# Optimization experiments

Hardware: AMD Instinct MI355X
Metric: run time of the kernel (lower is better)

## Reference

```python
import jax, jax.numpy as jnp
import numpy as np
import math

N = 16384
IN_F = 256
OUT_F = 64
EPS = 1e-6


def setup_inputs() -> dict:
    key = jax.random.key(0)
    k1, k2, k3, k4 = jax.random.split(key, 4)
    stdv = 1.0 / math.sqrt(OUT_F)
    inp = jax.random.normal(k1, (N, IN_F), dtype=jnp.float32)
    adj = jax.random.uniform(k2, (N, N), dtype=jnp.float32)
    weight = jax.random.uniform(k3, (IN_F, OUT_F), dtype=jnp.float32, minval=-stdv, maxval=stdv)
    bias = jax.random.uniform(k4, (OUT_F,), dtype=jnp.float32, minval=-stdv, maxval=stdv)
    return {"input": inp, "adj": adj, "weight": weight, "bias": bias, "p": 2}


def reference(input, adj, weight, bias, p):
    # support: [N, OUT_F]
    support = input @ weight
    mu = jnp.min(support)  # global scalar min
    pre_sup = support - mu + EPS  # >= EPS, safe for pow
    pre_top = pre_sup ** (p + 1)
    pre_down = pre_sup ** p
    # p-power mean aggregation: two adj matmuls sharing adj reads
    output = (adj @ pre_top) / (adj @ pre_down) + mu
    return output + bias
```

## Files before the change

### kernel.cpp

```cpp
#include <hip/hip_runtime.h>
#include <hip/hip_bf16.h>

typedef __attribute__((ext_vector_type(8))) short short8;
typedef __attribute__((ext_vector_type(4))) float f32x4;
typedef unsigned short u16;
typedef unsigned int u32;

#define NROWS 16384
#define KDIM 16384
#define EPS 1e-6f

__device__ __forceinline__ u16 f2bf(float x) {
    union { float f; u32 u; } v; v.f = x;
    u32 u = v.u;
    u32 r = (u + 0x7FFFu + ((u >> 16) & 1u)) >> 16;
    return (u16)r;
}

__device__ __forceinline__ void glds16(const void* g, void* l) {
    __builtin_amdgcn_global_load_lds(
        (const __attribute__((address_space(1))) void*)g,
        (__attribute__((address_space(3))) void*)l, 16, 0, 0);
}

__device__ __forceinline__ short cvbf(float x) {
    __hip_bfloat16 h = __float2bfloat16(x);
    return *(short*)&h;
}

__device__ __forceinline__ short8 cvt8(float4 a, float4 b) {
    short8 r = { cvbf(a.x), cvbf(a.y), cvbf(a.z), cvbf(a.w),
                 cvbf(b.x), cvbf(b.y), cvbf(b.z), cvbf(b.w) };
    return r;
}

__global__ __launch_bounds__(256) void wt_kernel(const float* __restrict__ W,
                                                 float* __restrict__ Wt) {
    int idx = blockIdx.x * 256 + threadIdx.x;
    int k = idx >> 6, c = idx & 63;
    Wt[c * 256 + k] = W[idx];
}

__global__ __launch_bounds__(256) void support_kernel(
    const float* __restrict__ inp, const float* __restrict__ Wt,
    float* __restrict__ sup)
{
    int tid = threadIdx.x;
    int col = tid & 63;
    int rr = tid >> 6;
    int rowbase = blockIdx.x * 32 + rr * 8;
    const float4* wt4 = (const float4*)(Wt + (size_t)col * 256);
    float acc[8];
#pragma unroll
    for (int i = 0; i < 8; ++i) acc[i] = 0.f;
    for (int k4 = 0; k4 < 64; ++k4) {
        float4 wv = wt4[k4];
#pragma unroll
        for (int i = 0; i < 8; ++i) {
            float4 iv = *((const float4*)(inp + (size_t)(rowbase + i) * 256) + k4);
            acc[i] += iv.x * wv.x + iv.y * wv.y + iv.z * wv.z + iv.w * wv.w;
        }
    }
#pragma unroll
    for (int i = 0; i < 8; ++i)
        sup[(size_t)(rowbase + i) * 64 + col] = acc[i];
}

__global__ __launch_bounds__(256) void min_part_kernel(
    const float* __restrict__ sup, float* __restrict__ partmin)
{
    __shared__ float wmin[4];
    int tid = threadIdx.x;
    const float4* s4 = (const float4*)sup;
    size_t idx = (size_t)blockIdx.x * 256 + tid;
    float m = 3.4e38f;
#pragma unroll
    for (int j = 0; j < 4; ++j) {
        float4 v = s4[idx + (size_t)j * 65536];
        m = fminf(m, fminf(fminf(v.x, v.y), fminf(v.z, v.w)));
    }
#pragma unroll
    for (int off = 32; off; off >>= 1) m = fminf(m, __shfl_down(m, off, 64));
    if ((tid & 63) == 0) wmin[tid >> 6] = m;
    __syncthreads();
    if (tid == 0)
        partmin[blockIdx.x] = fminf(fminf(wmin[0], wmin[1]), fminf(wmin[2], wmin[3]));
}

__global__ __launch_bounds__(256) void min_final_kernel(
    const float* __restrict__ partmin, float* __restrict__ mu)
{
    __shared__ float wmin[4];
    int tid = threadIdx.x;
    float m = partmin[tid];
#pragma unroll
    for (int off = 32; off; off >>= 1) m = fminf(m, __shfl_down(m, off, 64));
    if ((tid & 63) == 0) wmin[tid >> 6] = m;
    __syncthreads();
    if (tid == 0)
        mu[0] = fminf(fminf(wmin[0], wmin[1]), fminf(wmin[2], wmin[3]));
}

__global__ __launch_bounds__(256) void build_bt_kernel(
    const float* __restrict__ sup, const float* __restrict__ muptr,
    const int* __restrict__ pptr, u16* __restrict__ Bt)
{
    int k = blockIdx.x * 256 + threadIdx.x;
    float mu = *muptr;
    int p = *pptr;
    const float4* srow = (const float4*)(sup + (size_t)k * 64);
#pragma unroll
    for (int j = 0; j < 16; ++j) {
        float4 v = srow[j];
        float ss[4] = {v.x, v.y, v.z, v.w};
#pragma unroll
        for (int q = 0; q < 4; ++q) {
            int c = j * 4 + q;
            float s = ss[q] - mu + EPS;
            float d = 1.f;
            for (int i = 0; i < p; ++i) d *= s;
            Bt[(size_t)c * KDIM + k] = f2bf(d * s);
            Bt[(size_t)(c + 64) * KDIM + k] = f2bf(d);
        }
    }
}

#define BM 64
#define BN 128
#define BK 64
#define KH 8192
#define NTI 128

__global__ __launch_bounds__(512, 4) void gemm_kernel(
    const float* __restrict__ adj, const u16* __restrict__ Bt,
    float* __restrict__ Pp)
{
    __shared__ __align__(16) float Ash[2][BM * BK];
    __shared__ __align__(16) u16  Bsh[2][BN * BK];

    const int tid = threadIdx.x;
    const int rb = blockIdx.x >> 1;
    const int h  = blockIdx.x & 1;
    const size_t rowbase = (size_t)rb * BM;
    const size_t kbase = (size_t)h * KH;

    const int ga0 = tid,        ga1 = tid + 512;
    const int ar0 = ga0 >> 4,   ax0 = (ga0 & 15) ^ (ar0 & 7);
    const int ar1 = ga1 >> 4,   ax1 = (ga1 & 15) ^ (ar1 & 7);
    const float* asrc0 = adj + (rowbase + ar0) * KDIM + kbase + ax0 * 4;
    const float* asrc1 = adj + (rowbase + ar1) * KDIM + kbase + ax1 * 4;
    const int bn0 = ga0 >> 3,   bx0 = (ga0 & 7) ^ (bn0 & 7);
    const int bn1 = ga1 >> 3,   bx1 = (ga1 & 7) ^ (bn1 & 7);
    const u16* bsrc0 = Bt + (size_t)bn0 * KDIM + kbase + bx0 * 8;
    const u16* bsrc1 = Bt + (size_t)bn1 * KDIM + kbase + bx1 * 8;

    const int lane = tid & 63;
    const int w    = tid >> 6;
    const int wm   = w >> 1;
    const int wn   = w & 1;
    const int l15  = lane & 15, lg = lane >> 4;
    const int arow = wm * 16 + l15;
    const int asw  = arow & 7;

    f32x4 acc[4];
#pragma unroll
    for (int j = 0; j < 4; ++j) acc[j] = (f32x4){0.f, 0.f, 0.f, 0.f};

    auto stage = [&](int kt, int buf) {
        const int koff = kt * BK;
        char* ab = (char*)Ash[buf];
        char* bb = (char*)Bsh[buf];
        glds16(asrc0 + koff, ab + ga0 * 16);
        glds16(asrc1 + koff, ab + ga1 * 16);
        glds16(bsrc0 + koff, bb + ga0 * 16);
        glds16(bsrc1 + koff, bb + ga1 * 16);
    };

    stage(0, 0);

    for (int t = 0; t < NTI; ++t) {
        __syncthreads();
        if (t + 1 < NTI) stage(t + 1, (t + 1) & 1);
        const float4* As4 = (const float4*)Ash[t & 1];
        const short8* Bs8 = (const short8*)Bsh[t & 1];
#pragma unroll
        for (int ks = 0; ks < 2; ++ks) {
            const int x0 = ks * 8 + lg * 2;
            float4 fa = As4[arow * 16 + ((x0    ) ^ asw)];
            float4 fb = As4[arow * 16 + ((x0 + 1) ^ asw)];
            short8 a = cvt8(fa, fb);
            const int bx = ks * 4 + lg;
#pragma unroll
            for (int j = 0; j < 4; ++j) {
                const int n = wn * 32 + (j & 1) * 16 + (j >> 1) * 64 + l15;
                short8 b = Bs8[n * 8 + (bx ^ (n & 7))];
                acc[j] = __builtin_amdgcn_mfma_f32_16x16x32_bf16(a, b, acc[j], 0, 0, 0);
            }
        }
    }

    float* pb = Pp + (size_t)blockIdx.x * (BM * BN);
#pragma unroll
    for (int j = 0; j < 2; ++j) {
#pragma unroll
        for (int q = 0; q < 4; ++q) {
            int r = wm * 16 + lg * 4 + q;
            int c = wn * 32 + j * 16 + l15;
            pb[r * BN + c]      = acc[j][q];
            pb[r * BN + c + 64] = acc[j + 2][q];
        }
    }
}

__global__ __launch_bounds__(256) void reduce_kernel(
    const float* __restrict__ Pp, const float* __restrict__ bias,
    const float* __restrict__ muptr, float* __restrict__ out)
{
    int idx = blockIdx.x * 256 + threadIdx.x;
    int r = idx >> 6, c = idx & 63;
    int rb = r >> 6, rr = r & 63;
    const float* p0 = Pp + (size_t)(rb * 2) * (BM * BN) + rr * BN + c;
    const float* p1 = p0 + BM * BN;
    float T = p0[0]  + p1[0];
    float D = p0[64] + p1[64];
    out[idx] = T / D + muptr[0] + bias[c];
}

extern "C" void kernel_launch(void* const* d_in, const int* in_sizes, int n_in,
                              void* d_out, int out_size, void* d_ws, size_t ws_size,
                              hipStream_t stream)
{
    const float* inp  = (const float*)d_in[0];
    const float* adj  = (const float*)d_in[1];
    const float* W    = (const float*)d_in[2];
    const float* bias = (const float*)d_in[3];
    const int*   p    = (const int*)d_in[4];
    float* out = (float*)d_out;

    char* ws = (char*)d_ws;
    u16*   Bt      = (u16*)ws;
    float* partmin = (float*)(ws + (size_t)4 * 1024 * 1024);
    float* mu      = partmin + 256;
    float* Wt      = (float*)(ws + (size_t)4 * 1024 * 1024 + 4096);
    float* Pp      = (float*)(ws + (size_t)8 * 1024 * 1024);

    float* sup = out;

    wt_kernel       <<<64,   256, 0, stream>>>(W, Wt);
    support_kernel  <<<512,  256, 0, stream>>>(inp, Wt, sup);
    min_part_kernel <<<256,  256, 0, stream>>>(sup, partmin);
    min_final_kernel<<<1,    256, 0, stream>>>(partmin, mu);
    build_bt_kernel <<<64,   256, 0, stream>>>(sup, mu, p, Bt);
    gemm_kernel     <<<512,  512, 0, stream>>>(adj, Bt, Pp);
    reduce_kernel   <<<4096, 256, 0, stream>>>(Pp, bias, mu, out);
}
```

Before: 290.9 us.

## Enlarge GEMM row tile to 128 with 4 waves each computing 32x128

The adj GEMM now uses 128-row tiles with 256 threads per block, and each wave computes two 16-row fragments across all 128 B columns. This reuses each B fragment for two MFMAs and halves how often B is reloaded from global memory across blocks. The launch drops to 256 blocks of 256 threads, one per CU at most, which lowers occupancy and latency hiding on a kernel dominated by streaming adj. The partial-output layout and the reduce kernel are rewritten to index by row and K-half.

```diff
diff --git a/kernel.cpp b/kernel.cpp
--- a/kernel.cpp
+++ b/kernel.cpp
@@ -125,13 +125,13 @@
     }
 }
 
-#define BM 64
+#define BM 128
 #define BN 128
 #define BK 64
 #define KH 8192
 #define NTI 128
 
-__global__ __launch_bounds__(512, 4) void gemm_kernel(
+__global__ __launch_bounds__(256, 1) void gemm_kernel(
     const float* __restrict__ adj, const u16* __restrict__ Bt,
     float* __restrict__ Pp)
 {
@@ -139,41 +139,53 @@
     __shared__ __align__(16) u16  Bsh[2][BN * BK];
 
     const int tid = threadIdx.x;
-    const int rb = blockIdx.x >> 1;
+    const int rg = blockIdx.x >> 1;
     const int h  = blockIdx.x & 1;
-    const size_t rowbase = (size_t)rb * BM;
-    const size_t kbase = (size_t)h * KH;
-
-    const int ga0 = tid,        ga1 = tid + 512;
-    const int ar0 = ga0 >> 4,   ax0 = (ga0 & 15) ^ (ar0 & 7);
-    const int ar1 = ga1 >> 4,   ax1 = (ga1 & 15) ^ (ar1 & 7);
-    const float* asrc0 = adj + (rowbase + ar0) * KDIM + kbase + ax0 * 4;
-    const float* asrc1 = adj + (rowbase + ar1) * KDIM + kbase + ax1 * 4;
-    const int bn0 = ga0 >> 3,   bx0 = (ga0 & 7) ^ (bn0 & 7);
-    const int bn1 = ga1 >> 3,   bx1 = (ga1 & 7) ^ (bn1 & 7);
-    const u16* bsrc0 = Bt + (size_t)bn0 * KDIM + kbase + bx0 * 8;
-    const u16* bsrc1 = Bt + (size_t)bn1 * KDIM + kbase + bx1 * 8;
+    const size_t rowbase = (size_t)rg * BM;
+    const size_t kbase   = (size_t)h * KH;
+
+    const float* asp[8];
+#pragma unroll
+    for (int j = 0; j < 8; ++j) {
+        const int g = tid + j * 256;
+        const int ar = g >> 4;
+        const int ax = (g & 15) ^ (ar & 7);
+        asp[j] = adj + (rowbase + ar) * KDIM + kbase + ax * 4;
+    }
+    const u16* bsp[4];
+#pragma unroll
+    for (int j = 0; j < 4; ++j) {
+        const int g = tid + j * 256;
+        const int bn = g >> 3;
+        const int bx = (g & 7) ^ (bn & 7);
+        bsp[j] = Bt + (size_t)bn * KDIM + kbase + bx * 8;
+    }
 
     const int lane = tid & 63;
     const int w    = tid >> 6;
-    const int wm   = w >> 1;
-    const int wn   = w & 1;
     const int l15  = lane & 15, lg = lane >> 4;
-    const int arow = wm * 16 + l15;
-    const int asw  = arow & 7;
-
-    f32x4 acc[4];
-#pragma unroll
-    for (int j = 0; j < 4; ++j) acc[j] = (f32x4){0.f, 0.f, 0.f, 0.f};
+    const int arow0 = w * 32 + l15;
+    const int arow1 = arow0 + 16;
+    const int asw   = arow0 & 7;
+    const int bswl  = l15 & 7;
+
+    f32x4 acc0[8], acc1[8];
+#pragma unroll
+    for (int cf = 0; cf < 8; ++cf) {
+        acc0[cf] = (f32x4){0.f, 0.f, 0.f, 0.f};
+        acc1[cf] = acc0[cf];
+    }
 
     auto stage = [&](int kt, int buf) {
         const int koff = kt * BK;
         char* ab = (char*)Ash[buf];
         char* bb = (char*)Bsh[buf];
-        glds16(asrc0 + koff, ab + ga0 * 16);
-        glds16(asrc1 + koff, ab + ga1 * 16);
-        glds16(bsrc0 + koff, bb + ga0 * 16);
-        glds16(bsrc1 + koff, bb + ga1 * 16);
+#pragma unroll
+        for (int j = 0; j < 8; ++j)
+            glds16(asp[j] + koff, ab + (tid + j * 256) * 16);
+#pragma unroll
+        for (int j = 0; j < 4; ++j)
+            glds16(bsp[j] + koff, bb + (tid + j * 256) * 16);
     };
 
     stage(0, 0);
@@ -186,28 +198,32 @@
 #pragma unroll
         for (int ks = 0; ks < 2; ++ks) {
             const int x0 = ks * 8 + lg * 2;
-            float4 fa = As4[arow * 16 + ((x0    ) ^ asw)];
-            float4 fb = As4[arow * 16 + ((x0 + 1) ^ asw)];
-            short8 a = cvt8(fa, fb);
+            float4 fa0 = As4[arow0 * 16 + ((x0    ) ^ asw)];
+            float4 fa1 = As4[arow0 * 16 + ((x0 + 1) ^ asw)];
+            float4 fb0 = As4[arow1 * 16 + ((x0    ) ^ asw)];
+            float4 fb1 = As4[arow1 * 16 + ((x0 + 1) ^ asw)];
+            short8 a0 = cvt8(fa0, fa1);
+            short8 a1 = cvt8(fb0, fb1);
             const int bx = ks * 4 + lg;
 #pragma unroll
-            for (int j = 0; j < 4; ++j) {
-                const int n = wn * 32 + (j & 1) * 16 + (j >> 1) * 64 + l15;
-                short8 b = Bs8[n * 8 + (bx ^ (n & 7))];
-                acc[j] = __builtin_amdgcn_mfma_f32_16x16x32_bf16(a, b, acc[j], 0, 0, 0);
+            for (int cf = 0; cf < 8; ++cf) {
+                const int n = cf * 16 + l15;
+                short8 b = Bs8[n * 8 + (bx ^ bswl)];
+                acc0[cf] = __builtin_amdgcn_mfma_f32_16x16x32_bf16(a0, b, acc0[cf], 0, 0, 0);
+                acc1[cf] = __builtin_amdgcn_mfma_f32_16x16x32_bf16(a1, b, acc1[cf], 0, 0, 0);
             }
         }
     }
 
-    float* pb = Pp + (size_t)blockIdx.x * (BM * BN);
-#pragma unroll
-    for (int j = 0; j < 2; ++j) {
+    float* pb = Pp + ((size_t)h * NROWS + rowbase + w * 32) * 128;
+#pragma unroll
+    for (int cf = 0; cf < 8; ++cf) {
 #pragma unroll
         for (int q = 0; q < 4; ++q) {
-            int r = wm * 16 + lg * 4 + q;
-            int c = wn * 32 + j * 16 + l15;
-            pb[r * BN + c]      = acc[j][q];
-            pb[r * BN + c + 64] = acc[j + 2][q];
+            int r0 = lg * 4 + q;
+            int c  = cf * 16 + l15;
+            pb[(r0     ) * 128 + c] = acc0[cf][q];
+            pb[(r0 + 16) * 128 + c] = acc1[cf][q];
         }
     }
 }
@@ -218,11 +234,10 @@
 {
     int idx = blockIdx.x * 256 + threadIdx.x;
     int r = idx >> 6, c = idx & 63;
-    int rb = r >> 6, rr = r & 63;
-    const float* p0 = Pp + (size_t)(rb * 2) * (BM * BN) + rr * BN + c;
-    const float* p1 = p0 + BM * BN;
-    float T = p0[0]  + p1[0];
-    float D = p0[64] + p1[64];
+    const size_t qs = (size_t)NROWS * 128;
+    const float* p = Pp + (size_t)r * 128 + c;
+    float T = p[0]  + p[qs];
+    float D = p[64] + p[qs + 64];
     out[idx] = T / D + muptr[0] + bias[c];
 }
 
@@ -251,6 +266,6 @@
     min_part_kernel <<<256,  256, 0, stream>>>(sup, partmin);
     min_final_kernel<<<1,    256, 0, stream>>>(partmin, mu);
     build_bt_kernel <<<64,   256, 0, stream>>>(sup, mu, p, Bt);
-    gemm_kernel     <<<512,  512, 0, stream>>>(adj, Bt, Pp);
+    gemm_kernel     <<<256,  256, 0, stream>>>(adj, Bt, Pp);
     reduce_kernel   <<<4096, 256, 0, stream>>>(Pp, bias, mu, out);
 }
```

Result: slower. 448.3 us (+54.1%).
